# Optimization experiments

Measured on AMD Instinct MI355X. Metric: run time of the kernel, lower is better.

Reference implementation:

```python
import jax, jax.numpy as jnp
import numpy as np

B, n, A = 64, 1024, 32          # graphs, nodes/graph, actions/graph
N = B * n
EH = 2048                        # undirected edges per graph
HID, H = 128, 4
C = HID // H
NF, EF, AD, NI, L = 1, 1, 7, 4, 3
NEG_SLOPE = 0.2


def setup_inputs() -> dict:
    ks = jax.random.split(jax.random.key(0), 16)
    x = jax.random.normal(ks[0], (N, NF), jnp.float32)
    s = jax.random.randint(ks[1], (B, EH), 0, n)
    d = jax.random.randint(ks[2], (B, EH), 0, n)
    off = (jnp.arange(B) * n)[:, None]
    s = (s + off).reshape(-1)
    d = (d + off).reshape(-1)
    # bidirectional edges (unrooted trees): both i->j and j->i
    edge_index = jnp.stack([jnp.concatenate([s, d]), jnp.concatenate([d, s])]).astype(jnp.int32)
    E = edge_index.shape[1]
    edge_attr = jax.random.uniform(ks[3], (E, EF), jnp.float32)
    idx = jax.random.randint(ks[4], (B, A, NI), 0, n).astype(jnp.float32)
    meta = jax.random.normal(ks[5], (B, A, AD - NI), jnp.float32)
    action_tensor = jnp.concatenate([idx, meta], axis=-1)
    batch_idx = jnp.repeat(jnp.arange(B, dtype=jnp.int32), n)
    batch_ptr = jnp.arange(B + 1, dtype=jnp.int32) * n

    def lin(k, i, o):
        return jax.random.normal(k, (i, o), jnp.float32) / np.float32(np.sqrt(i))

    inp = dict(x=x, edge_attr=edge_attr, action_tensor=action_tensor,
               edge_index=edge_index, batch_idx=batch_idx, batch_ptr=batch_ptr)
    inp["Wn"] = lin(ks[6], NF, HID); inp["bn"] = jnp.zeros((HID,), jnp.float32)
    kl = jax.random.split(ks[7], 4 * L)
    inp["gWl"] = jnp.stack([lin(kl[i], HID, HID) for i in range(L)])
    inp["gWr"] = jnp.stack([lin(kl[L + i], HID, HID) for i in range(L)])
    inp["gWe"] = jnp.stack([lin(kl[2 * L + i], EF, HID) for i in range(L)])
    inp["gatt"] = jnp.stack([jax.random.normal(kl[3 * L + i], (H, C), jnp.float32) * 0.1 for i in range(L)])
    inp["gbl"] = jnp.zeros((L, HID), jnp.float32)
    inp["gbr"] = jnp.zeros((L, HID), jnp.float32)
    inp["gb"] = jnp.zeros((L, HID), jnp.float32)
    mlp_in = NI * HID + (AD - NI)
    inp["aW1"] = lin(ks[8], mlp_in, HID); inp["ab1"] = jnp.zeros((HID,), jnp.float32)
    inp["aW2"] = lin(ks[9], HID, HID); inp["ab2"] = jnp.zeros((HID,), jnp.float32)
    inp["qW1"] = lin(ks[10], 4 * HID, HID); inp["qb1"] = jnp.zeros((HID,), jnp.float32)
    inp["qW2"] = lin(ks[11], HID, HID); inp["qb2"] = jnp.zeros((HID,), jnp.float32)
    inp["qW3"] = lin(ks[12], HID, 1); inp["qb3"] = jnp.zeros((1,), jnp.float32)
    return inp


def _gatv2(h, src, dst, ea, Wl, bl, Wr, br, We, att, b):
    # PyG GATv2Conv: e_ij = att . leaky_relu(lin_l(x_j) + lin_r(x_i) + lin_edge(e_ij))
    Nn = h.shape[0]
    xl = (h @ Wl + bl).reshape(Nn, H, C)   # source transform
    xr = (h @ Wr + br).reshape(Nn, H, C)   # target transform
    ee = (ea @ We).reshape(-1, H, C)       # edge transform (no bias in PyG)
    e = jax.nn.leaky_relu(xl[src] + xr[dst] + ee, NEG_SLOPE)   # [E,H,C]
    logits = jnp.einsum('ehc,hc->eh', e, att)
    m = jax.ops.segment_max(logits, dst, num_segments=Nn)       # stable softmax per target node
    ex = jnp.exp(logits - m[dst])
    alpha = ex / jax.ops.segment_sum(ex, dst, num_segments=Nn)[dst]
    msg = (xl[src] * alpha[:, :, None]).reshape(-1, HID)
    return jax.ops.segment_sum(msg, dst, num_segments=Nn) + b


def reference(x, edge_attr, action_tensor, Wn, bn, gWl, gbl, gWr, gbr, gWe, gatt, gb,
              aW1, ab1, aW2, ab2, qW1, qb1, qW2, qb2, qW3, qb3,
              edge_index, batch_idx, batch_ptr):
    Nn = x.shape[0]
    nb = batch_ptr.shape[0] - 1
    # GATv2Conv default add_self_loops=True, fill_value='mean' for edge_attr
    loops = jnp.arange(Nn, dtype=edge_index.dtype)
    src = jnp.concatenate([edge_index[0], loops])
    dst = jnp.concatenate([edge_index[1], loops])
    ea = jnp.concatenate([edge_attr, jnp.broadcast_to(edge_attr.mean(0), (Nn, edge_attr.shape[1]))], 0)
    h = jax.nn.relu(x @ Wn + bn)
    for l in range(L):
        h = jax.nn.relu(_gatv2(h, src, dst, ea, gWl[l], gbl[l], gWr[l], gbr[l], gWe[l], gatt[l], gb[l])) + h
    # sum / mean / max pooling per graph
    sums = jax.ops.segment_sum(h, batch_idx, num_segments=nb)
    cnt = jax.ops.segment_sum(jnp.ones((Nn, 1), h.dtype), batch_idx, num_segments=nb)
    means = sums / cnt
    maxs = jax.ops.segment_max(h, batch_idx, num_segments=nb)
    tree_emb = jnp.concatenate([sums, means, maxs], -1)          # [B, 3*HID]
    # action encoding: gather node embeddings at action node indices (shifted by batch_ptr)
    ni = action_tensor[..., :NI].astype(jnp.int32) + batch_ptr[:-1][:, None, None]
    g = h[ni].reshape(nb, action_tensor.shape[1], NI * HID)
    ai = jnp.concatenate([g, action_tensor[..., NI:]], -1)
    ae = jax.nn.relu(jax.nn.relu(ai @ aW1 + ab1) @ aW2 + ab2)    # [B, A, HID]
    comb = jnp.concatenate([jnp.broadcast_to(tree_emb[:, None, :], (nb, ae.shape[1], 3 * HID)), ae], -1)
    q = jax.nn.relu(comb @ qW1 + qb1)
    q = jax.nn.relu(q @ qW2 + qb2)
    return (q @ qW3 + qb3).squeeze(-1)                            # [B, A]
```

## Files before the change

kernel.cpp:

```cpp
#include <hip/hip_runtime.h>
#include <hip/hip_bf16.h>

#define NNODES 65536
#define NGRAPH 64
#define NPG 1024
#define NACT 32
#define HID 128
#define DEGS 32

typedef __attribute__((ext_vector_type(8))) short bf16x8;
typedef __attribute__((ext_vector_type(4))) float f32x4;

__device__ __forceinline__ void load8(float* dst, const float* src) {
    float4 q0 = ((const float4*)src)[0];
    float4 q1 = ((const float4*)src)[1];
    dst[0]=q0.x; dst[1]=q0.y; dst[2]=q0.z; dst[3]=q0.w;
    dst[4]=q1.x; dst[5]=q1.y; dst[6]=q1.z; dst[7]=q1.w;
}

__device__ __forceinline__ void load4(float* dst, const float* src) {
    float4 q = *(const float4*)src;
    dst[0]=q.x; dst[1]=q.y; dst[2]=q.z; dst[3]=q.w;
}

__device__ __forceinline__ void load4bf(float* dst, const unsigned short* src) {
    uint2 q = *(const uint2*)src;
    dst[0] = __uint_as_float(q.x << 16); dst[1] = __uint_as_float(q.x & 0xffff0000u);
    dst[2] = __uint_as_float(q.y << 16); dst[3] = __uint_as_float(q.y & 0xffff0000u);
}

__device__ __forceinline__ unsigned short f2bf(float f) {
    unsigned int u = __float_as_uint(f);
    u = (u + 0x7fffu + ((u >> 16) & 1u)) >> 16;
    return (unsigned short)u;
}

__global__ void setup_k(const int* __restrict__ ei, const float* __restrict__ ea,
                        int* __restrict__ cursor, float* __restrict__ meansum,
                        int2* __restrict__ csr, int E0, int nsb,
                        const float* __restrict__ gWl, const float* __restrict__ gWr,
                        unsigned short* __restrict__ wtl, unsigned short* __restrict__ wtr,
                        const float* __restrict__ aW1, const float* __restrict__ aW2,
                        const float* __restrict__ qW1, const float* __restrict__ qW2,
                        unsigned short* __restrict__ wA1t, unsigned short* __restrict__ wA2t,
                        unsigned short* __restrict__ wQ1t, unsigned short* __restrict__ wQ2t) {
    int bid = blockIdx.x, t = threadIdx.x;
    if (bid < nsb) {
        __shared__ float s[256];
        int e = bid * 256 + t;
        float v = 0.f;
        if (e < E0) {
            int sn = ei[e], d = ei[E0 + e];
            int pos = atomicAdd(&cursor[d], 1);
            if (pos >= DEGS) pos = DEGS - 1;
            csr[(size_t)d * DEGS + pos] = make_int2(sn, __float_as_int(ea[e]));
            v = ea[e];
        }
        s[t] = v; __syncthreads();
        for (int off = 128; off > 0; off >>= 1) { if (t < off) s[t] += s[t+off]; __syncthreads(); }
        if (t == 0) atomicAdd(meansum, s[0]);
    } else if (bid < nsb + 192) {
        int idx = (bid - nsb) * 256 + t;
        int l = idx >> 14, rem = idx & 16383;
        int n = rem >> 7, k = rem & 127;
        int src = l*16384 + k*128 + n;
        wtl[idx] = f2bf(gWl[src]);
        wtr[idx] = f2bf(gWr[src]);
    } else {
        int n = bid - nsb - 192;
        for (int k = t; k < 544; k += 256)
            wA1t[n*544 + k] = (k < 515) ? f2bf(aW1[(size_t)k*128 + n]) : (unsigned short)0;
        if (t < 128) {
            wA2t[n*128 + t] = f2bf(aW2[(size_t)t*128 + n]);
            wQ1t[n*128 + t] = f2bf(qW1[(size_t)(384 + t)*128 + n]);
            wQ2t[n*128 + t] = f2bf(qW2[(size_t)t*128 + n]);
        }
    }
}

__global__ __launch_bounds__(256) void gemm_lr_mfma_k(
    const unsigned short* __restrict__ hb, const float* __restrict__ x,
    const float* __restrict__ Wn, const float* __restrict__ bn, int l0,
    const unsigned short* __restrict__ wtl, const unsigned short* __restrict__ wtr,
    const float* __restrict__ bl, const float* __restrict__ br,
    unsigned short* __restrict__ xlb, unsigned short* __restrict__ xrb) {
    int wave = threadIdx.x >> 6;
    int lane = threadIdx.x & 63;
    int lr = lane & 15;
    int lq = lane >> 4;
    int r0 = blockIdx.x * 128 + wave * 32;

    bf16x8 a[2][4];
    if (l0) {
        float xv0 = x[r0 + lr], xv1 = x[r0 + 16 + lr];
#pragma unroll
        for (int kf = 0; kf < 4; ++kf) {
            float wn[8], bv[8];
            load8(wn, Wn + kf*32 + lq*8);
            load8(bv, bn + kf*32 + lq*8);
            union { bf16x8 v; unsigned short u[8]; } p0, p1;
#pragma unroll
            for (int j = 0; j < 8; ++j) {
                p0.u[j] = f2bf(fmaxf(fmaf(xv0, wn[j], bv[j]), 0.f));
                p1.u[j] = f2bf(fmaxf(fmaf(xv1, wn[j], bv[j]), 0.f));
            }
            a[0][kf] = p0.v; a[1][kf] = p1.v;
        }
    } else {
        const short* hs = (const short*)hb;
#pragma unroll
        for (int rt = 0; rt < 2; ++rt)
#pragma unroll
            for (int kf = 0; kf < 4; ++kf)
                a[rt][kf] = *(const bf16x8*)(hs + (size_t)(r0 + rt*16 + lr)*HID + kf*32 + lq*8);
    }

    const short* ws[2]   = {(const short*)wtl, (const short*)wtr};
    const float* bias[2] = {bl, br};
    unsigned short* outp[2] = {xlb, xrb};

#pragma unroll
    for (int m = 0; m < 2; ++m) {
        const short* W = ws[m];
        f32x4 acc[2][8];
#pragma unroll
        for (int rt = 0; rt < 2; ++rt)
#pragma unroll
            for (int ct = 0; ct < 8; ++ct) acc[rt][ct] = (f32x4){0.f,0.f,0.f,0.f};

        bf16x8 b[4], nb[4];
#pragma unroll
        for (int kf = 0; kf < 4; ++kf)
            b[kf] = *(const bf16x8*)(W + (size_t)(lr)*HID + kf*32 + lq*8);
#pragma unroll
        for (int ct = 0; ct < 8; ++ct) {
            if (ct < 7) {
#pragma unroll
                for (int kf = 0; kf < 4; ++kf)
                    nb[kf] = *(const bf16x8*)(W + (size_t)((ct+1)*16 + lr)*HID + kf*32 + lq*8);
            }
#pragma unroll
            for (int rt = 0; rt < 2; ++rt)
#pragma unroll
                for (int kf = 0; kf < 4; ++kf)
                    acc[rt][ct] = __builtin_amdgcn_mfma_f32_16x16x32_bf16(a[rt][kf], b[kf], acc[rt][ct], 0, 0, 0);
#pragma unroll
            for (int kf = 0; kf < 4; ++kf) b[kf] = nb[kf];
        }
#pragma unroll
        for (int ct = 0; ct < 8; ++ct) {
            float bv = bias[m][ct*16 + lr];
#pragma unroll
            for (int rt = 0; rt < 2; ++rt)
#pragma unroll
                for (int rg = 0; rg < 4; ++rg) {
                    int row = r0 + rt*16 + lq*4 + rg;
                    outp[m][(size_t)row*HID + ct*16 + lr] = f2bf(acc[rt][ct][rg] + bv);
                }
        }
    }
}

__global__ __launch_bounds__(256, 6) void gat_edge_k(
    const unsigned short* __restrict__ xlb, const unsigned short* __restrict__ xrb,
    unsigned short* __restrict__ hb,
    const int* __restrict__ deg, const int2* __restrict__ csr,
    const float* __restrict__ We, const float* __restrict__ att,
    const float* __restrict__ gb, const float* __restrict__ meansum, float inv_e0,
    const float* __restrict__ x, const float* __restrict__ Wn, const float* __restrict__ bn,
    int l0, int do_pool, float* __restrict__ tree_sum, float* __restrict__ tree_max) {
    __shared__ float ps[8][132];
    __shared__ float pm[8][132];
    int xcd  = blockIdx.x & 7;
    int slot = blockIdx.x >> 3;
    int g    = xcd * 8 + (slot >> 7);
    int j    = slot & 127;
    int t    = threadIdx.x;
    int nd   = t >> 5;
    int v    = g * NPG + j * 8 + nd;
    int li   = t & 31;
    int base = li * 4;
    float mea = meansum[0] * inv_e0;

    float xrv[4], attv[4], wev[4];
    load4bf(xrv, xrb + (size_t)v*HID + base);
    load4(attv, att + base);
    load4(wev, We + base);

    float acc[4], xA[4];
    load4bf(xA, xlb + (size_t)v*HID + base);
    float m;
    {
        float lg = 0.f;
#pragma unroll
        for (int c = 0; c < 4; ++c) {
            float e = xA[c] + xrv[c] + mea * wev[c];
            e = fmaxf(e, 0.2f * e);
            lg = fmaf(attv[c], e, lg);
        }
        lg += __shfl_xor(lg, 1, 64);
        lg += __shfl_xor(lg, 2, 64);
        lg += __shfl_xor(lg, 4, 64);
        m = lg;
#pragma unroll
        for (int c = 0; c < 4; ++c) acc[c] = xA[c];
    }
    float den = 1.f;

    int dg = deg[v];
    if (dg > DEGS) dg = DEGS;
    if (dg > 0) {
        const int2* cp = csr + (size_t)v * DEGS;
        int2 e0 = cp[0];
        int2 e1 = cp[(1 < dg) ? 1 : dg - 1];
        float xB[4];
        load4bf(xA, xlb + (size_t)e0.x*HID + base);
        load4bf(xB, xlb + (size_t)e1.x*HID + base);
        for (int i = 0; i < dg; ++i) {
            int2 e2 = cp[(i + 2 < dg) ? i + 2 : dg - 1];
            float xC[4];
            load4bf(xC, xlb + (size_t)e2.x*HID + base);
            float an = __int_as_float(e0.y);

            float lg = 0.f;
#pragma unroll
            for (int c = 0; c < 4; ++c) {
                float e = xA[c] + xrv[c] + an * wev[c];
                e = fmaxf(e, 0.2f * e);
                lg = fmaf(attv[c], e, lg);
            }
            lg += __shfl_xor(lg, 1, 64);
            lg += __shfl_xor(lg, 2, 64);
            lg += __shfl_xor(lg, 4, 64);

            float mn  = fmaxf(m, lg);
            float sc  = __expf(m - mn);
            float wgt = __expf(lg - mn);
            den = den * sc + wgt;
#pragma unroll
            for (int c = 0; c < 4; ++c) acc[c] = acc[c] * sc + wgt * xA[c];
            m = mn;
            e0 = e1; e1 = e2;
#pragma unroll
            for (int c = 0; c < 4; ++c) { xA[c] = xB[c]; xB[c] = xC[c]; }
        }
    }

    float inv = 1.f / den;
    size_t o = (size_t)v*HID + base;
    float hold[4], gbv[4];
    if (l0) {
        float xv = x[v];
        float wn[4], bv[4];
        load4(wn, Wn + base);
        load4(bv, bn + base);
#pragma unroll
        for (int c = 0; c < 4; ++c) hold[c] = fmaxf(fmaf(xv, wn[c], bv[c]), 0.f);
    } else {
        load4bf(hold, hb + o);
    }
    load4(gbv, gb + base);
    float nh[4];
#pragma unroll
    for (int c = 0; c < 4; ++c) {
        float val = acc[c] * inv + gbv[c];
        val = val > 0.f ? val : 0.f;
        nh[c] = val + hold[c];
    }
    unsigned int* hbp = (unsigned int*)(hb + o);
    hbp[0] = (unsigned int)f2bf(nh[0]) | ((unsigned int)f2bf(nh[1]) << 16);
    hbp[1] = (unsigned int)f2bf(nh[2]) | ((unsigned int)f2bf(nh[3]) << 16);

    if (do_pool) {
#pragma unroll
        for (int c = 0; c < 4; ++c) { ps[nd][base + c] = nh[c]; pm[nd][base + c] = nh[c]; }
        __syncthreads();
        if (t < 128) {
            float s = 0.f;
#pragma unroll
            for (int n = 0; n < 8; ++n) s += ps[n][t];
            atomicAdd(&tree_sum[g*128 + t], s);
        } else {
            int col = t - 128;
            float mx = 0.f;
#pragma unroll
            for (int n = 0; n < 8; ++n) mx = fmaxf(mx, pm[n][col]);
            atomicMax((int*)&tree_max[g*128 + col], __float_as_int(mx));
        }
    }
}

#define SA1 552
#define SAC 136
__global__ __launch_bounds__(256) void action_q_k(
    const unsigned short* __restrict__ hb, const float* __restrict__ action,
    const int* __restrict__ batch_ptr,
    const float* __restrict__ tree_sum, const float* __restrict__ tree_max,
    const unsigned short* __restrict__ wA1t, const float* __restrict__ ab1,
    const unsigned short* __restrict__ wA2t, const float* __restrict__ ab2,
    const float* __restrict__ qW1, const unsigned short* __restrict__ wQ1t,
    const float* __restrict__ qb1,
    const unsigned short* __restrict__ wQ2t, const float* __restrict__ qb2,
    const float* __restrict__ qW3, const float* __restrict__ qb3,
    float* __restrict__ out) {
    int b = blockIdx.x;
    int t = threadIdx.x;
    int w  = t >> 6;
    int lane = t & 63;
    int lr = lane & 15;
    int lq = lane >> 4;

    __shared__ unsigned short aib[32 * SA1];
    __shared__ unsigned short z1s[32 * SAC];
    __shared__ unsigned short aes[32 * SAC];
    __shared__ unsigned short q1s[32 * SAC];
    __shared__ float q2f[32 * 132];
    __shared__ float tqA[128], tqB[128];
    __shared__ float psum[32][8];

    int ptr = batch_ptr[b];

    {
        int p = t >> 1, half = t & 1;
        int a = p >> 2, j = p & 3;
        const float* actp = action + (size_t)(b * NACT + a) * 7;
        int ni = (int)actp[j] + ptr;
        const uint4* src = (const uint4*)(hb + (size_t)ni * HID) + half * 8;
        uint4* dst = (uint4*)((char*)aib + ((size_t)a * SA1 + j * 128 + half * 64) * 2);
#pragma unroll
        for (int q = 0; q < 8; ++q) dst[q] = src[q];
        if (t < 32) {
            const float* ap = action + (size_t)(b * NACT + t) * 7;
            aib[t * SA1 + 512] = f2bf(ap[4]);
            aib[t * SA1 + 513] = f2bf(ap[5]);
            aib[t * SA1 + 514] = f2bf(ap[6]);
            for (int i = 3; i < 40; ++i) aib[t * SA1 + 512 + i] = 0;
        }
    }

    {
        if (t < 128) {
            int col = t;
            float acc = 0.f;
#pragma unroll 4
            for (int k = 0; k < 128; ++k) {
                float sv = tree_sum[b * 128 + k];
                acc = fmaf(sv, qW1[(size_t)k * 128 + col], acc);
                acc = fmaf(sv * (1.f / 1024.f), qW1[(size_t)(128 + k) * 128 + col], acc);
            }
            tqA[col] = acc;
        } else {
            int col = t - 128;
            float acc = 0.f;
#pragma unroll 4
            for (int k = 0; k < 128; ++k) {
                float mv = tree_max[b * 128 + k];
                acc = fmaf(mv, qW1[(size_t)(256 + k) * 128 + col], acc);
            }
            tqB[col] = acc;
        }
    }
    __syncthreads();

    f32x4 acc[2][2];
    const unsigned short* srcA;
    int strideA, K;

    srcA = aib; strideA = SA1; K = 544;
#pragma unroll
    for (int rt = 0; rt < 2; ++rt)
#pragma unroll
        for (int ci = 0; ci < 2; ++ci) acc[rt][ci] = (f32x4){0.f, 0.f, 0.f, 0.f};
    for (int ks = 0; ks < K; ks += 32) {
        bf16x8 a0 = *(const bf16x8*)(srcA + (0 * 16 + lr) * strideA + ks + lq * 8);
        bf16x8 a1 = *(const bf16x8*)(srcA + (1 * 16 + lr) * strideA + ks + lq * 8);
        bf16x8 b0 = *(const bf16x8*)(wA1t + (size_t)((2 * w + 0) * 16 + lr) * K + ks + lq * 8);
        bf16x8 b1 = *(const bf16x8*)(wA1t + (size_t)((2 * w + 1) * 16 + lr) * K + ks + lq * 8);
        acc[0][0] = __builtin_amdgcn_mfma_f32_16x16x32_bf16(a0, b0, acc[0][0], 0, 0, 0);
        acc[0][1] = __builtin_amdgcn_mfma_f32_16x16x32_bf16(a0, b1, acc[0][1], 0, 0, 0);
        acc[1][0] = __builtin_amdgcn_mfma_f32_16x16x32_bf16(a1, b0, acc[1][0], 0, 0, 0);
        acc[1][1] = __builtin_amdgcn_mfma_f32_16x16x32_bf16(a1, b1, acc[1][1], 0, 0, 0);
    }
#pragma unroll
    for (int ci = 0; ci < 2; ++ci) {
        int col = (2 * w + ci) * 16 + lr;
        float bv = ab1[col];
#pragma unroll
        for (int rt = 0; rt < 2; ++rt)
#pragma unroll
            for (int rg = 0; rg < 4; ++rg) {
                int row = rt * 16 + lq * 4 + rg;
                z1s[row * SAC + col] = f2bf(fmaxf(acc[rt][ci][rg] + bv, 0.f));
            }
    }
    __syncthreads();

    srcA = z1s; strideA = SAC; K = 128;
#pragma unroll
    for (int rt = 0; rt < 2; ++rt)
#pragma unroll
        for (int ci = 0; ci < 2; ++ci) acc[rt][ci] = (f32x4){0.f, 0.f, 0.f, 0.f};
#pragma unroll
    for (int ks = 0; ks < 128; ks += 32) {
        bf16x8 a0 = *(const bf16x8*)(srcA + (0 * 16 + lr) * strideA + ks + lq * 8);
        bf16x8 a1 = *(const bf16x8*)(srcA + (1 * 16 + lr) * strideA + ks + lq * 8);
        bf16x8 b0 = *(const bf16x8*)(wA2t + (size_t)((2 * w + 0) * 16 + lr) * K + ks + lq * 8);
        bf16x8 b1 = *(const bf16x8*)(wA2t + (size_t)((2 * w + 1) * 16 + lr) * K + ks + lq * 8);
        acc[0][0] = __builtin_amdgcn_mfma_f32_16x16x32_bf16(a0, b0, acc[0][0], 0, 0, 0);
        acc[0][1] = __builtin_amdgcn_mfma_f32_16x16x32_bf16(a0, b1, acc[0][1], 0, 0, 0);
        acc[1][0] = __builtin_amdgcn_mfma_f32_16x16x32_bf16(a1, b0, acc[1][0], 0, 0, 0);
        acc[1][1] = __builtin_amdgcn_mfma_f32_16x16x32_bf16(a1, b1, acc[1][1], 0, 0, 0);
    }
#pragma unroll
    for (int ci = 0; ci < 2; ++ci) {
        int col = (2 * w + ci) * 16 + lr;
        float bv = ab2[col];
#pragma unroll
        for (int rt = 0; rt < 2; ++rt)
#pragma unroll
            for (int rg = 0; rg < 4; ++rg) {
                int row = rt * 16 + lq * 4 + rg;
                aes[row * SAC + col] = f2bf(fmaxf(acc[rt][ci][rg] + bv, 0.f));
            }
    }
    __syncthreads();

    srcA = aes; strideA = SAC; K = 128;
#pragma unroll
    for (int rt = 0; rt < 2; ++rt)
#pragma unroll
        for (int ci = 0; ci < 2; ++ci) acc[rt][ci] = (f32x4){0.f, 0.f, 0.f, 0.f};
#pragma unroll
    for (int ks = 0; ks < 128; ks += 32) {
        bf16x8 a0 = *(const bf16x8*)(srcA + (0 * 16 + lr) * strideA + ks + lq * 8);
        bf16x8 a1 = *(const bf16x8*)(srcA + (1 * 16 + lr) * strideA + ks + lq * 8);
        bf16x8 b0 = *(const bf16x8*)(wQ1t + (size_t)((2 * w + 0) * 16 + lr) * K + ks + lq * 8);
        bf16x8 b1 = *(const bf16x8*)(wQ1t + (size_t)((2 * w + 1) * 16 + lr) * K + ks + lq * 8);
        acc[0][0] = __builtin_amdgcn_mfma_f32_16x16x32_bf16(a0, b0, acc[0][0], 0, 0, 0);
        acc[0][1] = __builtin_amdgcn_mfma_f32_16x16x32_bf16(a0, b1, acc[0][1], 0, 0, 0);
        acc[1][0] = __builtin_amdgcn_mfma_f32_16x16x32_bf16(a1, b0, acc[1][0], 0, 0, 0);
        acc[1][1] = __builtin_amdgcn_mfma_f32_16x16x32_bf16(a1, b1, acc[1][1], 0, 0, 0);
    }
#pragma unroll
    for (int ci = 0; ci < 2; ++ci) {
        int col = (2 * w + ci) * 16 + lr;
        float bv = qb1[col] + tqA[col] + tqB[col];
#pragma unroll
        for (int rt = 0; rt < 2; ++rt)
#pragma unroll
            for (int rg = 0; rg < 4; ++rg) {
                int row = rt * 16 + lq * 4 + rg;
                q1s[row * SAC + col] = f2bf(fmaxf(acc[rt][ci][rg] + bv, 0.f));
            }
    }
    __syncthreads();

    srcA = q1s; strideA = SAC; K = 128;
#pragma unroll
    for (int rt = 0; rt < 2; ++rt)
#pragma unroll
        for (int ci = 0; ci < 2; ++ci) acc[rt][ci] = (f32x4){0.f, 0.f, 0.f, 0.f};
#pragma unroll
    for (int ks = 0; ks < 128; ks += 32) {
        bf16x8 a0 = *(const bf16x8*)(srcA + (0 * 16 + lr) * strideA + ks + lq * 8);
        bf16x8 a1 = *(const bf16x8*)(srcA + (1 * 16 + lr) * strideA + ks + lq * 8);
        bf16x8 b0 = *(const bf16x8*)(wQ2t + (size_t)((2 * w + 0) * 16 + lr) * K + ks + lq * 8);
        bf16x8 b1 = *(const bf16x8*)(wQ2t + (size_t)((2 * w + 1) * 16 + lr) * K + ks + lq * 8);
        acc[0][0] = __builtin_amdgcn_mfma_f32_16x16x32_bf16(a0, b0, acc[0][0], 0, 0, 0);
        acc[0][1] = __builtin_amdgcn_mfma_f32_16x16x32_bf16(a0, b1, acc[0][1], 0, 0, 0);
        acc[1][0] = __builtin_amdgcn_mfma_f32_16x16x32_bf16(a1, b0, acc[1][0], 0, 0, 0);
        acc[1][1] = __builtin_amdgcn_mfma_f32_16x16x32_bf16(a1, b1, acc[1][1], 0, 0, 0);
    }
#pragma unroll
    for (int ci = 0; ci < 2; ++ci) {
        int col = (2 * w + ci) * 16 + lr;
        float bv = qb2[col];
#pragma unroll
        for (int rt = 0; rt < 2; ++rt)
#pragma unroll
            for (int rg = 0; rg < 4; ++rg) {
                int row = rt * 16 + lq * 4 + rg;
                q2f[row * 132 + col] = fmaxf(acc[rt][ci][rg] + bv, 0.f);
            }
    }
    __syncthreads();

    {
        int a = t >> 3, seg = t & 7;
        float s = 0.f;
#pragma unroll
        for (int k = 0; k < 16; ++k)
            s = fmaf(q2f[a * 132 + seg * 16 + k], qW3[seg * 16 + k], s);
        psum[a][seg] = s;
    }
    __syncthreads();
    if (t < 32) {
        float s = qb3[0];
#pragma unroll
        for (int i = 0; i < 8; ++i) s += psum[t][i];
        out[(size_t)b * NACT + t] = s;
    }
}

extern "C" void kernel_launch(void* const* d_in, const int* in_sizes, int n_in,
                              void* d_out, int out_size, void* d_ws, size_t ws_size,
                              hipStream_t stream) {
    const float* x         = (const float*)d_in[0];
    const float* edge_attr = (const float*)d_in[1];
    const float* action    = (const float*)d_in[2];
    const int*   edge_idx  = (const int*)d_in[3];
    const int*   batch_ptr = (const int*)d_in[5];
    const float* Wn  = (const float*)d_in[6];
    const float* bn  = (const float*)d_in[7];
    const float* gWl = (const float*)d_in[8];
    const float* gWr = (const float*)d_in[9];
    const float* gWe = (const float*)d_in[10];
    const float* gatt= (const float*)d_in[11];
    const float* gbl = (const float*)d_in[12];
    const float* gbr = (const float*)d_in[13];
    const float* gb  = (const float*)d_in[14];
    const float* aW1 = (const float*)d_in[15];
    const float* ab1 = (const float*)d_in[16];
    const float* aW2 = (const float*)d_in[17];
    const float* ab2 = (const float*)d_in[18];
    const float* qW1 = (const float*)d_in[19];
    const float* qb1 = (const float*)d_in[20];
    const float* qW2 = (const float*)d_in[21];
    const float* qb2 = (const float*)d_in[22];
    const float* qW3 = (const float*)d_in[23];
    const float* qb3 = (const float*)d_in[24];
    float* out = (float*)d_out;

    const int E0 = in_sizes[1];
    const int N  = NNODES;

    char* w = (char*)d_ws;
    auto alloc = [&](size_t bytes) { void* p = (void*)w; w += (bytes + 255) & ~(size_t)255; return p; };
    unsigned short* hb  = (unsigned short*)alloc((size_t)N * HID * 2);
    unsigned short* xlb = (unsigned short*)alloc((size_t)N * HID * 2);
    unsigned short* xrb = (unsigned short*)alloc((size_t)N * HID * 2);
    int2*  csr      = (int2*)alloc((size_t)N * DEGS * 8);
    int*   cursor   = (int*)alloc((size_t)N * 4);
    float* meansum  = (float*)alloc(256);
    float* tree_sum = (float*)alloc((size_t)NGRAPH * 128 * 4);
    float* tree_max = (float*)alloc((size_t)NGRAPH * 128 * 4);
    size_t zero_span = (size_t)((char*)(tree_max + NGRAPH * 128) - (char*)cursor);
    unsigned short* wtl = (unsigned short*)alloc((size_t)3*128*128*2);
    unsigned short* wtr = (unsigned short*)alloc((size_t)3*128*128*2);
    unsigned short* wA1t = (unsigned short*)alloc((size_t)128*544*2);
    unsigned short* wA2t = (unsigned short*)alloc((size_t)128*128*2);
    unsigned short* wQ1t = (unsigned short*)alloc((size_t)128*128*2);
    unsigned short* wQ2t = (unsigned short*)alloc((size_t)128*128*2);

    hipMemsetAsync(cursor, 0, zero_span, stream);

    int nsb = (E0 + 255) / 256;
    setup_k<<<nsb + 320, 256, 0, stream>>>(edge_idx, edge_attr, cursor, meansum, csr, E0, nsb,
                                           gWl, gWr, wtl, wtr,
                                           aW1, aW2, qW1, qW2, wA1t, wA2t, wQ1t, wQ2t);

    float inv_e0 = 1.0f / (float)E0;
    for (int l = 0; l < 3; ++l) {
        gemm_lr_mfma_k<<<N / 128, 256, 0, stream>>>(
            hb, x, Wn, bn, (l == 0) ? 1 : 0,
            wtl + (size_t)l*128*128, wtr + (size_t)l*128*128,
            gbl + l*HID, gbr + l*HID, xlb, xrb);
        gat_edge_k<<<N / 8, 256, 0, stream>>>(
            xlb, xrb, hb, cursor, csr,
            gWe + l*HID, gatt + l*128, gb + l*HID, meansum, inv_e0,
            x, Wn, bn, (l == 0) ? 1 : 0, (l == 2) ? 1 : 0, tree_sum, tree_max);
    }

    action_q_k<<<NGRAPH, 256, 0, stream>>>(
        hb, action, batch_ptr, tree_sum, tree_max,
        wA1t, ab1, wA2t, ab2, qW1, wQ1t, qb1, wQ2t, qb2, qW3, qb3, out);
}
```

Baseline: 316.6 us.

## Fuse all GAT layers, pooling and action head into one per-graph kernel

Replaces the per-layer GEMM and edge kernels plus the action kernel with a single 1024-thread block per graph. Each block builds its own CSR in shared memory with a prefix scan, removing the global atomic CSR build and the degree cap. It then runs all three layers and the pooling in-block, synchronising with barriers instead of kernel boundaries. This removes about seven launches and the global scatter, but leaves only 64 blocks, far fewer than the GPU has compute units, so parallelism is much lower.

```diff
diff --git a/kernel.cpp b/kernel.cpp
--- a/kernel.cpp
+++ b/kernel.cpp
@@ -6,7 +6,7 @@
 #define NPG 1024
 #define NACT 32
 #define HID 128
-#define DEGS 32
+#define SAC 136
 
 typedef __attribute__((ext_vector_type(8))) short bf16x8;
 typedef __attribute__((ext_vector_type(4))) float f32x4;
@@ -35,9 +35,7 @@
     return (unsigned short)u;
 }
 
-__global__ void setup_k(const int* __restrict__ ei, const float* __restrict__ ea,
-                        int* __restrict__ cursor, float* __restrict__ meansum,
-                        int2* __restrict__ csr, int E0, int nsb,
+__global__ void setup_k(const float* __restrict__ ea, float* __restrict__ meansum, int E0, int nmb,
                         const float* __restrict__ gWl, const float* __restrict__ gWr,
                         unsigned short* __restrict__ wtl, unsigned short* __restrict__ wtr,
                         const float* __restrict__ aW1, const float* __restrict__ aW2,
@@ -45,29 +43,22 @@
                         unsigned short* __restrict__ wA1t, unsigned short* __restrict__ wA2t,
                         unsigned short* __restrict__ wQ1t, unsigned short* __restrict__ wQ2t) {
     int bid = blockIdx.x, t = threadIdx.x;
-    if (bid < nsb) {
+    if (bid < nmb) {
         __shared__ float s[256];
         int e = bid * 256 + t;
-        float v = 0.f;
-        if (e < E0) {
-            int sn = ei[e], d = ei[E0 + e];
-            int pos = atomicAdd(&cursor[d], 1);
-            if (pos >= DEGS) pos = DEGS - 1;
-            csr[(size_t)d * DEGS + pos] = make_int2(sn, __float_as_int(ea[e]));
-            v = ea[e];
-        }
-        s[t] = v; __syncthreads();
+        s[t] = (e < E0) ? ea[e] : 0.f;
+        __syncthreads();
         for (int off = 128; off > 0; off >>= 1) { if (t < off) s[t] += s[t+off]; __syncthreads(); }
         if (t == 0) atomicAdd(meansum, s[0]);
-    } else if (bid < nsb + 192) {
-        int idx = (bid - nsb) * 256 + t;
+    } else if (bid < nmb + 192) {
+        int idx = (bid - nmb) * 256 + t;
         int l = idx >> 14, rem = idx & 16383;
         int n = rem >> 7, k = rem & 127;
         int src = l*16384 + k*128 + n;
         wtl[idx] = f2bf(gWl[src]);
         wtr[idx] = f2bf(gWr[src]);
     } else {
-        int n = bid - nsb - 192;
+        int n = bid - nmb - 192;
         for (int k = t; k < 544; k += 256)
             wA1t[n*544 + k] = (k < 515) ? f2bf(aW1[(size_t)k*128 + n]) : (unsigned short)0;
         if (t < 128) {
@@ -78,427 +69,354 @@
     }
 }
 
-__global__ __launch_bounds__(256) void gemm_lr_mfma_k(
-    const unsigned short* __restrict__ hb, const float* __restrict__ x,
-    const float* __restrict__ Wn, const float* __restrict__ bn, int l0,
+__global__ __launch_bounds__(1024) void mega_k(
+    const float* __restrict__ x, const int* __restrict__ ei, const float* __restrict__ ea,
+    const float* __restrict__ action, const int* __restrict__ batch_ptr,
+    const float* __restrict__ Wn, const float* __restrict__ bn,
     const unsigned short* __restrict__ wtl, const unsigned short* __restrict__ wtr,
-    const float* __restrict__ bl, const float* __restrict__ br,
-    unsigned short* __restrict__ xlb, unsigned short* __restrict__ xrb) {
-    int wave = threadIdx.x >> 6;
-    int lane = threadIdx.x & 63;
-    int lr = lane & 15;
-    int lq = lane >> 4;
-    int r0 = blockIdx.x * 128 + wave * 32;
-
-    bf16x8 a[2][4];
-    if (l0) {
-        float xv0 = x[r0 + lr], xv1 = x[r0 + 16 + lr];
-#pragma unroll
-        for (int kf = 0; kf < 4; ++kf) {
-            float wn[8], bv[8];
-            load8(wn, Wn + kf*32 + lq*8);
-            load8(bv, bn + kf*32 + lq*8);
-            union { bf16x8 v; unsigned short u[8]; } p0, p1;
-#pragma unroll
-            for (int j = 0; j < 8; ++j) {
-                p0.u[j] = f2bf(fmaxf(fmaf(xv0, wn[j], bv[j]), 0.f));
-                p1.u[j] = f2bf(fmaxf(fmaf(xv1, wn[j], bv[j]), 0.f));
-            }
-            a[0][kf] = p0.v; a[1][kf] = p1.v;
-        }
-    } else {
-        const short* hs = (const short*)hb;
-#pragma unroll
-        for (int rt = 0; rt < 2; ++rt)
-#pragma unroll
-            for (int kf = 0; kf < 4; ++kf)
-                a[rt][kf] = *(const bf16x8*)(hs + (size_t)(r0 + rt*16 + lr)*HID + kf*32 + lq*8);
-    }
-
-    const short* ws[2]   = {(const short*)wtl, (const short*)wtr};
-    const float* bias[2] = {bl, br};
-    unsigned short* outp[2] = {xlb, xrb};
-
-#pragma unroll
-    for (int m = 0; m < 2; ++m) {
-        const short* W = ws[m];
-        f32x4 acc[2][8];
-#pragma unroll
-        for (int rt = 0; rt < 2; ++rt)
-#pragma unroll
-            for (int ct = 0; ct < 8; ++ct) acc[rt][ct] = (f32x4){0.f,0.f,0.f,0.f};
-
-        bf16x8 b[4], nb[4];
-#pragma unroll
-        for (int kf = 0; kf < 4; ++kf)
-            b[kf] = *(const bf16x8*)(W + (size_t)(lr)*HID + kf*32 + lq*8);
-#pragma unroll
-        for (int ct = 0; ct < 8; ++ct) {
-            if (ct < 7) {
-#pragma unroll
-                for (int kf = 0; kf < 4; ++kf)
-                    nb[kf] = *(const bf16x8*)(W + (size_t)((ct+1)*16 + lr)*HID + kf*32 + lq*8);
-            }
-#pragma unroll
-            for (int rt = 0; rt < 2; ++rt)
-#pragma unroll
-                for (int kf = 0; kf < 4; ++kf)
-                    acc[rt][ct] = __builtin_amdgcn_mfma_f32_16x16x32_bf16(a[rt][kf], b[kf], acc[rt][ct], 0, 0, 0);
-#pragma unroll
-            for (int kf = 0; kf < 4; ++kf) b[kf] = nb[kf];
-        }
-#pragma unroll
-        for (int ct = 0; ct < 8; ++ct) {
-            float bv = bias[m][ct*16 + lr];
-#pragma unroll
-            for (int rt = 0; rt < 2; ++rt)
-#pragma unroll
-                for (int rg = 0; rg < 4; ++rg) {
-                    int row = r0 + rt*16 + lq*4 + rg;
-                    outp[m][(size_t)row*HID + ct*16 + lr] = f2bf(acc[rt][ct][rg] + bv);
-                }
-        }
-    }
-}
-
-__global__ __launch_bounds__(256, 6) void gat_edge_k(
-    const unsigned short* __restrict__ xlb, const unsigned short* __restrict__ xrb,
-    unsigned short* __restrict__ hb,
-    const int* __restrict__ deg, const int2* __restrict__ csr,
-    const float* __restrict__ We, const float* __restrict__ att,
-    const float* __restrict__ gb, const float* __restrict__ meansum, float inv_e0,
-    const float* __restrict__ x, const float* __restrict__ Wn, const float* __restrict__ bn,
-    int l0, int do_pool, float* __restrict__ tree_sum, float* __restrict__ tree_max) {
-    __shared__ float ps[8][132];
-    __shared__ float pm[8][132];
-    int xcd  = blockIdx.x & 7;
-    int slot = blockIdx.x >> 3;
-    int g    = xcd * 8 + (slot >> 7);
-    int j    = slot & 127;
-    int t    = threadIdx.x;
-    int nd   = t >> 5;
-    int v    = g * NPG + j * 8 + nd;
-    int li   = t & 31;
-    int base = li * 4;
-    float mea = meansum[0] * inv_e0;
-
-    float xrv[4], attv[4], wev[4];
-    load4bf(xrv, xrb + (size_t)v*HID + base);
-    load4(attv, att + base);
-    load4(wev, We + base);
-
-    float acc[4], xA[4];
-    load4bf(xA, xlb + (size_t)v*HID + base);
-    float m;
-    {
-        float lg = 0.f;
-#pragma unroll
-        for (int c = 0; c < 4; ++c) {
-            float e = xA[c] + xrv[c] + mea * wev[c];
-            e = fmaxf(e, 0.2f * e);
-            lg = fmaf(attv[c], e, lg);
-        }
-        lg += __shfl_xor(lg, 1, 64);
-        lg += __shfl_xor(lg, 2, 64);
-        lg += __shfl_xor(lg, 4, 64);
-        m = lg;
-#pragma unroll
-        for (int c = 0; c < 4; ++c) acc[c] = xA[c];
-    }
-    float den = 1.f;
-
-    int dg = deg[v];
-    if (dg > DEGS) dg = DEGS;
-    if (dg > 0) {
-        const int2* cp = csr + (size_t)v * DEGS;
-        int2 e0 = cp[0];
-        int2 e1 = cp[(1 < dg) ? 1 : dg - 1];
-        float xB[4];
-        load4bf(xA, xlb + (size_t)e0.x*HID + base);
-        load4bf(xB, xlb + (size_t)e1.x*HID + base);
-        for (int i = 0; i < dg; ++i) {
-            int2 e2 = cp[(i + 2 < dg) ? i + 2 : dg - 1];
-            float xC[4];
-            load4bf(xC, xlb + (size_t)e2.x*HID + base);
-            float an = __int_as_float(e0.y);
-
-            float lg = 0.f;
-#pragma unroll
-            for (int c = 0; c < 4; ++c) {
-                float e = xA[c] + xrv[c] + an * wev[c];
-                e = fmaxf(e, 0.2f * e);
-                lg = fmaf(attv[c], e, lg);
-            }
-            lg += __shfl_xor(lg, 1, 64);
-            lg += __shfl_xor(lg, 2, 64);
-            lg += __shfl_xor(lg, 4, 64);
-
-            float mn  = fmaxf(m, lg);
-            float sc  = __expf(m - mn);
-            float wgt = __expf(lg - mn);
-            den = den * sc + wgt;
-#pragma unroll
-            for (int c = 0; c < 4; ++c) acc[c] = acc[c] * sc + wgt * xA[c];
-            m = mn;
-            e0 = e1; e1 = e2;
-#pragma unroll
-            for (int c = 0; c < 4; ++c) { xA[c] = xB[c]; xB[c] = xC[c]; }
-        }
-    }
-
-    float inv = 1.f / den;
-    size_t o = (size_t)v*HID + base;
-    float hold[4], gbv[4];
-    if (l0) {
-        float xv = x[v];
-        float wn[4], bv[4];
-        load4(wn, Wn + base);
-        load4(bv, bn + base);
-#pragma unroll
-        for (int c = 0; c < 4; ++c) hold[c] = fmaxf(fmaf(xv, wn[c], bv[c]), 0.f);
-    } else {
-        load4bf(hold, hb + o);
-    }
-    load4(gbv, gb + base);
-    float nh[4];
-#pragma unroll
-    for (int c = 0; c < 4; ++c) {
-        float val = acc[c] * inv + gbv[c];
-        val = val > 0.f ? val : 0.f;
-        nh[c] = val + hold[c];
-    }
-    unsigned int* hbp = (unsigned int*)(hb + o);
-    hbp[0] = (unsigned int)f2bf(nh[0]) | ((unsigned int)f2bf(nh[1]) << 16);
-    hbp[1] = (unsigned int)f2bf(nh[2]) | ((unsigned int)f2bf(nh[3]) << 16);
-
-    if (do_pool) {
-#pragma unroll
-        for (int c = 0; c < 4; ++c) { ps[nd][base + c] = nh[c]; pm[nd][base + c] = nh[c]; }
-        __syncthreads();
-        if (t < 128) {
-            float s = 0.f;
-#pragma unroll
-            for (int n = 0; n < 8; ++n) s += ps[n][t];
-            atomicAdd(&tree_sum[g*128 + t], s);
-        } else {
-            int col = t - 128;
-            float mx = 0.f;
-#pragma unroll
-            for (int n = 0; n < 8; ++n) mx = fmaxf(mx, pm[n][col]);
-            atomicMax((int*)&tree_max[g*128 + col], __float_as_int(mx));
-        }
-    }
-}
-
-#define SA1 552
-#define SAC 136
-__global__ __launch_bounds__(256) void action_q_k(
-    const unsigned short* __restrict__ hb, const float* __restrict__ action,
-    const int* __restrict__ batch_ptr,
-    const float* __restrict__ tree_sum, const float* __restrict__ tree_max,
+    const float* __restrict__ gbl, const float* __restrict__ gbr,
+    const float* __restrict__ gWe, const float* __restrict__ gatt, const float* __restrict__ gbb,
+    const float* __restrict__ meansum, float inv_e0,
     const unsigned short* __restrict__ wA1t, const float* __restrict__ ab1,
     const unsigned short* __restrict__ wA2t, const float* __restrict__ ab2,
     const float* __restrict__ qW1, const unsigned short* __restrict__ wQ1t,
     const float* __restrict__ qb1,
     const unsigned short* __restrict__ wQ2t, const float* __restrict__ qb2,
     const float* __restrict__ qW3, const float* __restrict__ qb3,
-    float* __restrict__ out) {
-    int b = blockIdx.x;
-    int t = threadIdx.x;
-    int w  = t >> 6;
-    int lane = t & 63;
-    int lr = lane & 15;
-    int lq = lane >> 4;
-
-    __shared__ unsigned short aib[32 * SA1];
-    __shared__ unsigned short z1s[32 * SAC];
-    __shared__ unsigned short aes[32 * SAC];
-    __shared__ unsigned short q1s[32 * SAC];
-    __shared__ float q2f[32 * 132];
-    __shared__ float tqA[128], tqB[128];
-    __shared__ float psum[32][8];
-
-    int ptr = batch_ptr[b];
+    unsigned short* __restrict__ xlb, unsigned short* __restrict__ xrb,
+    unsigned short* __restrict__ hb, float* __restrict__ out, int E0) {
+
+    __shared__ __align__(16) char smem[46592];
+    __shared__ float tree_s[128], tree_m[128], tqA[128], tqB[128];
+    unsigned short* s_src = (unsigned short*)smem;
+    float*          s_ea  = (float*)(smem + 8192);
+    int*            s_deg = (int*)(smem + 24576);
+    int*            s_row = (int*)(smem + 28672);
+    int*            s_cur = (int*)(smem + 32768);
+    unsigned short* z1s  = (unsigned short*)smem;
+    unsigned short* aes  = (unsigned short*)(smem + 8704);
+    unsigned short* q1s  = (unsigned short*)(smem + 17408);
+    float*          q2f  = (float*)(smem + 26112);
+    float*          psum = (float*)(smem + 43008);
+    int*            s_ni = (int*)(smem + 44032);
+    unsigned short* amt  = (unsigned short*)(smem + 44544);
+
+    int g  = blockIdx.x;
+    int t  = threadIdx.x;
+    int nb = g * NPG;
+    int wave = t >> 6, lane = t & 63, lr = lane & 15, lq = lane >> 4;
+
+    s_deg[t] = 0; s_cur[t] = 0;
+    if (t < 128) { tree_s[t] = 0.f; tree_m[t] = 0.f; }
+    __syncthreads();
+    int edl[4]; unsigned short esl[4]; float eav[4];
+#pragma unroll
+    for (int k = 0; k < 4; ++k) {
+        int eloc = k * 1024 + t;
+        int c = (eloc < 2048) ? g*2048 + eloc : (E0 >> 1) + g*2048 + (eloc - 2048);
+        esl[k] = (unsigned short)(ei[c] - nb);
+        edl[k] = ei[E0 + c] - nb;
+        eav[k] = ea[c];
+        atomicAdd(&s_deg[edl[k]], 1);
+    }
+    __syncthreads();
+    s_row[t] = s_deg[t]; __syncthreads();
+    for (int off = 1; off < 1024; off <<= 1) {
+        int v = (t >= off) ? s_row[t - off] : 0; __syncthreads();
+        s_row[t] += v; __syncthreads();
+    }
+    int excl = s_row[t] - s_deg[t]; __syncthreads();
+    s_row[t] = excl; __syncthreads();
+#pragma unroll
+    for (int k = 0; k < 4; ++k) {
+        int pos = atomicAdd(&s_cur[edl[k]], 1);
+        int slot = s_row[edl[k]] + pos;
+        s_src[slot] = esl[k];
+        s_ea[slot]  = eav[k];
+    }
+    __syncthreads();
+
+    float mea = meansum[0] * inv_e0;
+
+    for (int l = 0; l < 3; ++l) {
+        const short* Wl = (const short*)(wtl + (size_t)l*16384);
+        const short* Wr = (const short*)(wtr + (size_t)l*16384);
+        const float* blp = gbl + l*128;
+        const float* brp = gbr + l*128;
+        const short* hs = (const short*)hb;
+        for (int rep = 0; rep < 4; ++rep) {
+            int r0 = rep * 256 + wave * 16;
+            bf16x8 afr[4];
+            if (l == 0) {
+                float xv = x[nb + r0 + lr];
+#pragma unroll
+                for (int kf = 0; kf < 4; ++kf) {
+                    float wn[8], bv[8];
+                    load8(wn, Wn + kf*32 + lq*8);
+                    load8(bv, bn + kf*32 + lq*8);
+                    union { bf16x8 v; unsigned short u[8]; } p;
+#pragma unroll
+                    for (int j2 = 0; j2 < 8; ++j2)
+                        p.u[j2] = f2bf(fmaxf(fmaf(xv, wn[j2], bv[j2]), 0.f));
+                    afr[kf] = p.v;
+                }
+            } else {
+#pragma unroll
+                for (int kf = 0; kf < 4; ++kf)
+                    afr[kf] = *(const bf16x8*)(hs + (size_t)(nb + r0 + lr)*HID + kf*32 + lq*8);
+            }
+#pragma unroll
+            for (int m = 0; m < 2; ++m) {
+                const short* W = m ? Wr : Wl;
+                const float* bias = m ? brp : blp;
+                unsigned short* outp = m ? xrb : xlb;
+                f32x4 acc[8];
+#pragma unroll
+                for (int ct = 0; ct < 8; ++ct) acc[ct] = (f32x4){0.f,0.f,0.f,0.f};
+                bf16x8 b[4], nb2[4];
+#pragma unroll
+                for (int kf = 0; kf < 4; ++kf)
+                    b[kf] = *(const bf16x8*)(W + (size_t)lr*HID + kf*32 + lq*8);
+#pragma unroll
+                for (int ct = 0; ct < 8; ++ct) {
+                    if (ct < 7) {
+#pragma unroll
+                        for (int kf = 0; kf < 4; ++kf)
+                            nb2[kf] = *(const bf16x8*)(W + (size_t)((ct+1)*16 + lr)*HID + kf*32 + lq*8);
+                    }
+#pragma unroll
+                    for (int kf = 0; kf < 4; ++kf)
+                        acc[ct] = __builtin_amdgcn_mfma_f32_16x16x32_bf16(afr[kf], b[kf], acc[ct], 0, 0, 0);
+#pragma unroll
+                    for (int kf = 0; kf < 4; ++kf) b[kf] = nb2[kf];
+                }
+#pragma unroll
+                for (int ct = 0; ct < 8; ++ct) {
+                    float bv = bias[ct*16 + lr];
+#pragma unroll
+                    for (int rg = 0; rg < 4; ++rg) {
+                        int row = nb + r0 + lq*4 + rg;
+                        outp[(size_t)row*HID + ct*16 + lr] = f2bf(acc[ct][rg] + bv);
+                    }
+                }
+            }
+        }
+        __syncthreads();
+
+        int li = t & 31, base4 = li * 4, grp = t >> 5;
+        float attv[4], wev[4], gbv[4];
+        load4(attv, gatt + l*128 + base4);
+        load4(wev,  gWe  + l*128 + base4);
+        load4(gbv,  gbb  + l*128 + base4);
+        float rs[4] = {0.f,0.f,0.f,0.f}, rm[4] = {0.f,0.f,0.f,0.f};
+        for (int iter = 0; iter < 32; ++iter) {
+            int vl = iter * 32 + grp;
+            int v  = nb + vl;
+            float xrv[4];
+            load4bf(xrv, xrb + (size_t)v*HID + base4);
+            float acc[4], xA[4];
+            load4bf(xA, xlb + (size_t)v*HID + base4);
+            float m;
+            {
+                float lg = 0.f;
+#pragma unroll
+                for (int c = 0; c < 4; ++c) {
+                    float e = xA[c] + xrv[c] + mea * wev[c];
+                    e = fmaxf(e, 0.2f * e);
+                    lg = fmaf(attv[c], e, lg);
+                }
+                lg += __shfl_xor(lg, 1, 64);
+                lg += __shfl_xor(lg, 2, 64);
+                lg += __shfl_xor(lg, 4, 64);
+                m = lg;
+#pragma unroll
+                for (int c = 0; c < 4; ++c) acc[c] = xA[c];
+            }
+            float den = 1.f;
+            int s0 = s_row[vl], dg = s_deg[vl];
+            if (dg > 0) {
+                int sl0 = s_src[s0];
+                int sl1 = s_src[s0 + ((1 < dg) ? 1 : 0)];
+                float xB[4];
+                load4bf(xA, xlb + (size_t)(nb + sl0)*HID + base4);
+                load4bf(xB, xlb + (size_t)(nb + sl1)*HID + base4);
+                for (int i = 0; i < dg; ++i) {
+                    int sl2 = s_src[s0 + ((i + 2 < dg) ? i + 2 : dg - 1)];
+                    float xC[4];
+                    load4bf(xC, xlb + (size_t)(nb + sl2)*HID + base4);
+                    float an = s_ea[s0 + i];
+
+                    float lg = 0.f;
+#pragma unroll
+                    for (int c = 0; c < 4; ++c) {
+                        float e = xA[c] + xrv[c] + an * wev[c];
+                        e = fmaxf(e, 0.2f * e);
+                        lg = fmaf(attv[c], e, lg);
+                    }
+                    lg += __shfl_xor(lg, 1, 64);
+                    lg += __shfl_xor(lg, 2, 64);
+                    lg += __shfl_xor(lg, 4, 64);
+
+                    float mn  = fmaxf(m, lg);
+                    float sc  = __expf(m - mn);
+                    float wgt = __expf(lg - mn);
+                    den = den * sc + wgt;
+#pragma unroll
+                    for (int c = 0; c < 4; ++c) acc[c] = acc[c] * sc + wgt * xA[c];
+                    m = mn;
+#pragma unroll
+                    for (int c = 0; c < 4; ++c) { xA[c] = xB[c]; xB[c] = xC[c]; }
+                }
+            }
+            float inv = 1.f / den;
+            size_t o = (size_t)v*HID + base4;
+            float hold[4];
+            if (l == 0) {
+                float xv = x[v];
+                float wn[4], bv[4];
+                load4(wn, Wn + base4);
+                load4(bv, bn + base4);
+#pragma unroll
+                for (int c = 0; c < 4; ++c) hold[c] = fmaxf(fmaf(xv, wn[c], bv[c]), 0.f);
+            } else {
+                load4bf(hold, hb + o);
+            }
+            float nh[4];
+#pragma unroll
+            for (int c = 0; c < 4; ++c) {
+                float val = acc[c] * inv + gbv[c];
+                val = val > 0.f ? val : 0.f;
+                nh[c] = val + hold[c];
+            }
+            unsigned int* hbp = (unsigned int*)(hb + o);
+            hbp[0] = (unsigned int)f2bf(nh[0]) | ((unsigned int)f2bf(nh[1]) << 16);
+            hbp[1] = (unsigned int)f2bf(nh[2]) | ((unsigned int)f2bf(nh[3]) << 16);
+            if (l == 2) {
+#pragma unroll
+                for (int c = 0; c < 4; ++c) { rs[c] += nh[c]; rm[c] = fmaxf(rm[c], nh[c]); }
+            }
+        }
+        if (l == 2) {
+#pragma unroll
+            for (int c = 0; c < 4; ++c) {
+                atomicAdd(&tree_s[base4 + c], rs[c]);
+                atomicMax((int*)&tree_m[base4 + c], __float_as_int(rm[c]));
+            }
+        }
+        __syncthreads();
+    }
+
+    int ptr = batch_ptr[g];
+    if (t < 128) {
+        int a = t >> 2, j = t & 3;
+        s_ni[t] = (int)action[(size_t)(g*NACT + a)*7 + j] + ptr;
+    } else if (t < 160) {
+        int a = t - 128;
+        const float* ap = action + (size_t)(g*NACT + a)*7;
+        amt[a*32 + 0] = f2bf(ap[4]);
+        amt[a*32 + 1] = f2bf(ap[5]);
+        amt[a*32 + 2] = f2bf(ap[6]);
+        for (int i = 3; i < 32; ++i) amt[a*32 + i] = 0;
+    }
+    if (t < 128) {
+        int col = t;
+        float acc = 0.f;
+#pragma unroll 4
+        for (int k = 0; k < 128; ++k) {
+            float sv = tree_s[k];
+            acc = fmaf(sv, qW1[(size_t)k*128 + col], acc);
+            acc = fmaf(sv * (1.f/1024.f), qW1[(size_t)(128 + k)*128 + col], acc);
+        }
+        tqA[col] = acc;
+    } else if (t < 256) {
+        int col = t - 128;
+        float acc = 0.f;
+#pragma unroll 4
+        for (int k = 0; k < 128; ++k)
+            acc = fmaf(tree_m[k], qW1[(size_t)(256 + k)*128 + col], acc);
+        tqB[col] = acc;
+    }
+    __syncthreads();
+
+    int rt = wave & 1, ci = wave >> 1;
+    int a_row = rt*16 + lr;
+    int colq  = ci*16 + lr;
 
     {
-        int p = t >> 1, half = t & 1;
-        int a = p >> 2, j = p & 3;
-        const float* actp = action + (size_t)(b * NACT + a) * 7;
-        int ni = (int)actp[j] + ptr;
-        const uint4* src = (const uint4*)(hb + (size_t)ni * HID) + half * 8;
-        uint4* dst = (uint4*)((char*)aib + ((size_t)a * SA1 + j * 128 + half * 64) * 2);
-#pragma unroll
-        for (int q = 0; q < 8; ++q) dst[q] = src[q];
-        if (t < 32) {
-            const float* ap = action + (size_t)(b * NACT + t) * 7;
-            aib[t * SA1 + 512] = f2bf(ap[4]);
-            aib[t * SA1 + 513] = f2bf(ap[5]);
-            aib[t * SA1 + 514] = f2bf(ap[6]);
-            for (int i = 3; i < 40; ++i) aib[t * SA1 + 512 + i] = 0;
-        }
-    }
-
+        f32x4 acc = (f32x4){0.f,0.f,0.f,0.f};
+        for (int ks = 0; ks < 544; ks += 32) {
+            bf16x8 av;
+            if (ks < 512) {
+                int ni = s_ni[a_row*4 + (ks >> 7)];
+                av = *(const bf16x8*)((const short*)hb + (size_t)ni*HID + (ks & 127) + lq*8);
+            } else {
+                av = *(const bf16x8*)(amt + a_row*32 + lq*8);
+            }
+            bf16x8 bv = *(const bf16x8*)(wA1t + (size_t)colq*544 + ks + lq*8);
+            acc = __builtin_amdgcn_mfma_f32_16x16x32_bf16(av, bv, acc, 0, 0, 0);
+        }
+        float bv = ab1[colq];
+#pragma unroll
+        for (int rg = 0; rg < 4; ++rg)
+            z1s[(rt*16 + lq*4 + rg)*SAC + colq] = f2bf(fmaxf(acc[rg] + bv, 0.f));
+    }
+    __syncthreads();
     {
-        if (t < 128) {
-            int col = t;
-            float acc = 0.f;
-#pragma unroll 4
-            for (int k = 0; k < 128; ++k) {
-                float sv = tree_sum[b * 128 + k];
-                acc = fmaf(sv, qW1[(size_t)k * 128 + col], acc);
-                acc = fmaf(sv * (1.f / 1024.f), qW1[(size_t)(128 + k) * 128 + col], acc);
-            }
-            tqA[col] = acc;
-        } else {
-            int col = t - 128;
-            float acc = 0.f;
-#pragma unroll 4
-            for (int k = 0; k < 128; ++k) {
-                float mv = tree_max[b * 128 + k];
-                acc = fmaf(mv, qW1[(size_t)(256 + k) * 128 + col], acc);
-            }
-            tqB[col] = acc;
-        }
-    }
-    __syncthreads();
-
-    f32x4 acc[2][2];
-    const unsigned short* srcA;
-    int strideA, K;
-
-    srcA = aib; strideA = SA1; K = 544;
-#pragma unroll
-    for (int rt = 0; rt < 2; ++rt)
-#pragma unroll
-        for (int ci = 0; ci < 2; ++ci) acc[rt][ci] = (f32x4){0.f, 0.f, 0.f, 0.f};
-    for (int ks = 0; ks < K; ks += 32) {
-        bf16x8 a0 = *(const bf16x8*)(srcA + (0 * 16 + lr) * strideA + ks + lq * 8);
-        bf16x8 a1 = *(const bf16x8*)(srcA + (1 * 16 + lr) * strideA + ks + lq * 8);
-        bf16x8 b0 = *(const bf16x8*)(wA1t + (size_t)((2 * w + 0) * 16 + lr) * K + ks + lq * 8);
-        bf16x8 b1 = *(const bf16x8*)(wA1t + (size_t)((2 * w + 1) * 16 + lr) * K + ks + lq * 8);
-        acc[0][0] = __builtin_amdgcn_mfma_f32_16x16x32_bf16(a0, b0, acc[0][0], 0, 0, 0);
-        acc[0][1] = __builtin_amdgcn_mfma_f32_16x16x32_bf16(a0, b1, acc[0][1], 0, 0, 0);
-        acc[1][0] = __builtin_amdgcn_mfma_f32_16x16x32_bf16(a1, b0, acc[1][0], 0, 0, 0);
-        acc[1][1] = __builtin_amdgcn_mfma_f32_16x16x32_bf16(a1, b1, acc[1][1], 0, 0, 0);
-    }
-#pragma unroll
-    for (int ci = 0; ci < 2; ++ci) {
-        int col = (2 * w + ci) * 16 + lr;
-        float bv = ab1[col];
-#pragma unroll
-        for (int rt = 0; rt < 2; ++rt)
-#pragma unroll
-            for (int rg = 0; rg < 4; ++rg) {
-                int row = rt * 16 + lq * 4 + rg;
-                z1s[row * SAC + col] = f2bf(fmaxf(acc[rt][ci][rg] + bv, 0.f));
-            }
-    }
-    __syncthreads();
-
-    srcA = z1s; strideA = SAC; K = 128;
-#pragma unroll
-    for (int rt = 0; rt < 2; ++rt)
-#pragma unroll
-        for (int ci = 0; ci < 2; ++ci) acc[rt][ci] = (f32x4){0.f, 0.f, 0.f, 0.f};
-#pragma unroll
-    for (int ks = 0; ks < 128; ks += 32) {
-        bf16x8 a0 = *(const bf16x8*)(srcA + (0 * 16 + lr) * strideA + ks + lq * 8);
-        bf16x8 a1 = *(const bf16x8*)(srcA + (1 * 16 + lr) * strideA + ks + lq * 8);
-        bf16x8 b0 = *(const bf16x8*)(wA2t + (size_t)((2 * w + 0) * 16 + lr) * K + ks + lq * 8);
-        bf16x8 b1 = *(const bf16x8*)(wA2t + (size_t)((2 * w + 1) * 16 + lr) * K + ks + lq * 8);
-        acc[0][0] = __builtin_amdgcn_mfma_f32_16x16x32_bf16(a0, b0, acc[0][0], 0, 0, 0);
-        acc[0][1] = __builtin_amdgcn_mfma_f32_16x16x32_bf16(a0, b1, acc[0][1], 0, 0, 0);
-        acc[1][0] = __builtin_amdgcn_mfma_f32_16x16x32_bf16(a1, b0, acc[1][0], 0, 0, 0);
-        acc[1][1] = __builtin_amdgcn_mfma_f32_16x16x32_bf16(a1, b1, acc[1][1], 0, 0, 0);
-    }
-#pragma unroll
-    for (int ci = 0; ci < 2; ++ci) {
-        int col = (2 * w + ci) * 16 + lr;
-        float bv = ab2[col];
-#pragma unroll
-        for (int rt = 0; rt < 2; ++rt)
-#pragma unroll
-            for (int rg = 0; rg < 4; ++rg) {
-                int row = rt * 16 + lq * 4 + rg;
-                aes[row * SAC + col] = f2bf(fmaxf(acc[rt][ci][rg] + bv, 0.f));
-            }
-    }
-    __syncthreads();
-
-    srcA = aes; strideA = SAC; K = 128;
-#pragma unroll
-    for (int rt = 0; rt < 2; ++rt)
-#pragma unroll
-        for (int ci = 0; ci < 2; ++ci) acc[rt][ci] = (f32x4){0.f, 0.f, 0.f, 0.f};
-#pragma unroll
-    for (int ks = 0; ks < 128; ks += 32) {
-        bf16x8 a0 = *(const bf16x8*)(srcA + (0 * 16 + lr) * strideA + ks + lq * 8);
-        bf16x8 a1 = *(const bf16x8*)(srcA + (1 * 16 + lr) * strideA + ks + lq * 8);
-        bf16x8 b0 = *(const bf16x8*)(wQ1t + (size_t)((2 * w + 0) * 16 + lr) * K + ks + lq * 8);
-        bf16x8 b1 = *(const bf16x8*)(wQ1t + (size_t)((2 * w + 1) * 16 + lr) * K + ks + lq * 8);
-        acc[0][0] = __builtin_amdgcn_mfma_f32_16x16x32_bf16(a0, b0, acc[0][0], 0, 0, 0);
-        acc[0][1] = __builtin_amdgcn_mfma_f32_16x16x32_bf16(a0, b1, acc[0][1], 0, 0, 0);
-        acc[1][0] = __builtin_amdgcn_mfma_f32_16x16x32_bf16(a1, b0, acc[1][0], 0, 0, 0);
-        acc[1][1] = __builtin_amdgcn_mfma_f32_16x16x32_bf16(a1, b1, acc[1][1], 0, 0, 0);
-    }
-#pragma unroll
-    for (int ci = 0; ci < 2; ++ci) {
-        int col = (2 * w + ci) * 16 + lr;
-        float bv = qb1[col] + tqA[col] + tqB[col];
-#pragma unroll
-        for (int rt = 0; rt < 2; ++rt)
-#pragma unroll
-            for (int rg = 0; rg < 4; ++rg) {
-                int row = rt * 16 + lq * 4 + rg;
-                q1s[row * SAC + col] = f2bf(fmaxf(acc[rt][ci][rg] + bv, 0.f));
-            }
-    }
-    __syncthreads();
-
-    srcA = q1s; strideA = SAC; K = 128;
-#pragma unroll
-    for (int rt = 0; rt < 2; ++rt)
-#pragma unroll
-        for (int ci = 0; ci < 2; ++ci) acc[rt][ci] = (f32x4){0.f, 0.f, 0.f, 0.f};
-#pragma unroll
-    for (int ks = 0; ks < 128; ks += 32) {
-        bf16x8 a0 = *(const bf16x8*)(srcA + (0 * 16 + lr) * strideA + ks + lq * 8);
-        bf16x8 a1 = *(const bf16x8*)(srcA + (1 * 16 + lr) * strideA + ks + lq * 8);
-        bf16x8 b0 = *(const bf16x8*)(wQ2t + (size_t)((2 * w + 0) * 16 + lr) * K + ks + lq * 8);
-        bf16x8 b1 = *(const bf16x8*)(wQ2t + (size_t)((2 * w + 1) * 16 + lr) * K + ks + lq * 8);
-        acc[0][0] = __builtin_amdgcn_mfma_f32_16x16x32_bf16(a0, b0, acc[0][0], 0, 0, 0);
-        acc[0][1] = __builtin_amdgcn_mfma_f32_16x16x32_bf16(a0, b1, acc[0][1], 0, 0, 0);
-        acc[1][0] = __builtin_amdgcn_mfma_f32_16x16x32_bf16(a1, b0, acc[1][0], 0, 0, 0);
-        acc[1][1] = __builtin_amdgcn_mfma_f32_16x16x32_bf16(a1, b1, acc[1][1], 0, 0, 0);
-    }
-#pragma unroll
-    for (int ci = 0; ci < 2; ++ci) {
-        int col = (2 * w + ci) * 16 + lr;
-        float bv = qb2[col];
-#pragma unroll
-        for (int rt = 0; rt < 2; ++rt)
-#pragma unroll
-            for (int rg = 0; rg < 4; ++rg) {
-                int row = rt * 16 + lq * 4 + rg;
-                q2f[row * 132 + col] = fmaxf(acc[rt][ci][rg] + bv, 0.f);
-            }
-    }
-    __syncthreads();
-
+        f32x4 acc = (f32x4){0.f,0.f,0.f,0.f};
+#pragma unroll
+        for (int ks = 0; ks < 128; ks += 32) {
+            bf16x8 av = *(const bf16x8*)(z1s + a_row*SAC + ks + lq*8);
+            bf16x8 bv = *(const bf16x8*)(wA2t + (size_t)colq*128 + ks + lq*8);
+            acc = __builtin_amdgcn_mfma_f32_16x16x32_bf16(av, bv, acc, 0, 0, 0);
+        }
+        float bv = ab2[colq];
+#pragma unroll
+        for (int rg = 0; rg < 4; ++rg)
+            aes[(rt*16 + lq*4 + rg)*SAC + colq] = f2bf(fmaxf(acc[rg] + bv, 0.f));
+    }
+    __syncthreads();
     {
+        f32x4 acc = (f32x4){0.f,0.f,0.f,0.f};
+#pragma unroll
+        for (int ks = 0; ks < 128; ks += 32) {
+            bf16x8 av = *(const bf16x8*)(aes + a_row*SAC + ks + lq*8);
+            bf16x8 bv = *(const bf16x8*)(wQ1t + (size_t)colq*128 + ks + lq*8);
+            acc = __builtin_amdgcn_mfma_f32_16x16x32_bf16(av, bv, acc, 0, 0, 0);
+        }
+        float bv = qb1[colq] + tqA[colq] + tqB[colq];
+#pragma unroll
+        for (int rg = 0; rg < 4; ++rg)
+            q1s[(rt*16 + lq*4 + rg)*SAC + colq] = f2bf(fmaxf(acc[rg] + bv, 0.f));
+    }
+    __syncthreads();
+    {
+        f32x4 acc = (f32x4){0.f,0.f,0.f,0.f};
+#pragma unroll
+        for (int ks = 0; ks < 128; ks += 32) {
+            bf16x8 av = *(const bf16x8*)(q1s + a_row*SAC + ks + lq*8);
+            bf16x8 bv = *(const bf16x8*)(wQ2t + (size_t)colq*128 + ks + lq*8);
+            acc = __builtin_amdgcn_mfma_f32_16x16x32_bf16(av, bv, acc, 0, 0, 0);
+        }
+        float bv = qb2[colq];
+#pragma unroll
+        for (int rg = 0; rg < 4; ++rg)
+            q2f[(rt*16 + lq*4 + rg)*132 + colq] = fmaxf(acc[rg] + bv, 0.f);
+    }
+    __syncthreads();
+    if (t < 256) {
         int a = t >> 3, seg = t & 7;
         float s = 0.f;
 #pragma unroll
         for (int k = 0; k < 16; ++k)
-            s = fmaf(q2f[a * 132 + seg * 16 + k], qW3[seg * 16 + k], s);
-        psum[a][seg] = s;
+            s = fmaf(q2f[a*132 + seg*16 + k], qW3[seg*16 + k], s);
+        psum[a*8 + seg] = s;
     }
     __syncthreads();
     if (t < 32) {
         float s = qb3[0];
 #pragma unroll
-        for (int i = 0; i < 8; ++i) s += psum[t][i];
-        out[(size_t)b * NACT + t] = s;
+        for (int i = 0; i < 8; ++i) s += psum[t*8 + i];
+        out[(size_t)g*NACT + t] = s;
     }
 }
 
@@ -539,12 +457,7 @@
     unsigned short* hb  = (unsigned short*)alloc((size_t)N * HID * 2);
     unsigned short* xlb = (unsigned short*)alloc((size_t)N * HID * 2);
     unsigned short* xrb = (unsigned short*)alloc((size_t)N * HID * 2);
-    int2*  csr      = (int2*)alloc((size_t)N * DEGS * 8);
-    int*   cursor   = (int*)alloc((size_t)N * 4);
-    float* meansum  = (float*)alloc(256);
-    float* tree_sum = (float*)alloc((size_t)NGRAPH * 128 * 4);
-    float* tree_max = (float*)alloc((size_t)NGRAPH * 128 * 4);
-    size_t zero_span = (size_t)((char*)(tree_max + NGRAPH * 128) - (char*)cursor);
+    float* meansum      = (float*)alloc(256);
     unsigned short* wtl = (unsigned short*)alloc((size_t)3*128*128*2);
     unsigned short* wtr = (unsigned short*)alloc((size_t)3*128*128*2);
     unsigned short* wA1t = (unsigned short*)alloc((size_t)128*544*2);
@@ -552,26 +465,18 @@
     unsigned short* wQ1t = (unsigned short*)alloc((size_t)128*128*2);
     unsigned short* wQ2t = (unsigned short*)alloc((size_t)128*128*2);
 
-    hipMemsetAsync(cursor, 0, zero_span, stream);
-
-    int nsb = (E0 + 255) / 256;
-    setup_k<<<nsb + 320, 256, 0, stream>>>(edge_idx, edge_attr, cursor, meansum, csr, E0, nsb,
+    hipMemsetAsync(meansum, 0, 4, stream);
+
+    int nmb = (E0 + 255) / 256;
+    setup_k<<<nmb + 320, 256, 0, stream>>>(edge_attr, meansum, E0, nmb,
                                            gWl, gWr, wtl, wtr,
                                            aW1, aW2, qW1, qW2, wA1t, wA2t, wQ1t, wQ2t);
 
     float inv_e0 = 1.0f / (float)E0;
-    for (int l = 0; l < 3; ++l) {
-        gemm_lr_mfma_k<<<N / 128, 256, 0, stream>>>(
-            hb, x, Wn, bn, (l == 0) ? 1 : 0,
-            wtl + (size_t)l*128*128, wtr + (size_t)l*128*128,
-            gbl + l*HID, gbr + l*HID, xlb, xrb);
-        gat_edge_k<<<N / 8, 256, 0, stream>>>(
-            xlb, xrb, hb, cursor, csr,
-            gWe + l*HID, gatt + l*128, gb + l*HID, meansum, inv_e0,
-            x, Wn, bn, (l == 0) ? 1 : 0, (l == 2) ? 1 : 0, tree_sum, tree_max);
-    }
-
-    action_q_k<<<NGRAPH, 256, 0, stream>>>(
-        hb, action, batch_ptr, tree_sum, tree_max,
-        wA1t, ab1, wA2t, ab2, qW1, wQ1t, qb1, wQ2t, qb2, qW3, qb3, out);
-}
+    mega_k<<<NGRAPH, 1024, 0, stream>>>(
+        x, edge_idx, edge_attr, action, batch_ptr,
+        Wn, bn, wtl, wtr, gbl, gbr, gWe, gatt, gb,
+        meansum, inv_e0,
+        wA1t, ab1, wA2t, ab2, qW1, wQ1t, qb1, wQ2t, qb2, qW3, qb3,
+        xlb, xrb, hb, out, E0);
+}
```

New measurement: 963.9 us. 204% more time.
